# Kernel optimization log

Measured on AMD Instinct MI355X. Metric: run time of the kernel, lower is better.

The kernel has to match this reference:

```python
import jax, jax.numpy as jnp
import numpy as np

N_FEAT = 350; D = 512; L = 4; DS = 64; NREG = 6; REG_E = 32
B = 32; S = 2048
CLAMP = 20.0


def _ln(x, g, b, eps=1e-5):
    mu = jnp.mean(x, axis=-1, keepdims=True)
    var = jnp.mean(jnp.square(x - mu), axis=-1, keepdims=True)
    return (x - mu) * jax.lax.rsqrt(var + eps) * g + b


def _slstm(x, ln_g, ln_b, Wi, bi, Wf, bf, Wz, bz, Wo, bo, Wp, bp):
    # x: [B,S,D] -> out: [B,S,D]
    xn = _ln(x, ln_g, ln_b)
    log_i = jnp.clip(jnp.einsum('bsd,de->bse', xn, Wi) + bi, -CLAMP, CLAMP)
    log_f = jnp.clip(jnp.einsum('bsd,de->bse', xn, Wf) + bf, -CLAMP, CLAMP)
    z = jnp.tanh(jnp.einsum('bsd,de->bse', xn, Wz) + bz)
    o = jax.nn.sigmoid(jnp.einsum('bsd,de->bse', xn, Wo) + bo)

    def step(carry, inp):
        m, c = carry
        li, lf, zt, ot = inp
        m_new = jnp.maximum(m + lf, li)
        i_s = jnp.exp(li - m_new)
        f_s = jnp.exp(m + lf - m_new)
        c_new = f_s * c + i_s * zt
        h = ot * jnp.tanh(c_new)
        return (m_new, c_new), h

    bsz = x.shape[0]
    init = (jnp.zeros((bsz, DS), x.dtype), jnp.zeros((bsz, DS), x.dtype))
    seq = (jnp.swapaxes(log_i, 0, 1), jnp.swapaxes(log_f, 0, 1),
           jnp.swapaxes(z, 0, 1), jnp.swapaxes(o, 0, 1))
    _, hs = jax.lax.scan(step, init, seq)  # hs: [S,B,DS]
    hs = jnp.swapaxes(hs, 0, 1)  # [B,S,DS]
    return jnp.einsum('bse,ed->bsd', hs, Wp) + bp


def setup_inputs() -> dict:
    key = jax.random.key(0)
    ks = iter(jax.random.split(key, 64))
    def p(*shape):
        return jax.random.normal(next(ks), shape, dtype=jnp.float32) * 0.02
    return {
        'x': jax.random.normal(next(ks), (B, S, N_FEAT), dtype=jnp.float32),
        'regime_ids': jax.random.randint(next(ks), (B, S), 0, NREG),
        'emb_regime': p(NREG, REG_E),
        'grn_w1': p(N_FEAT + REG_E, D), 'grn_b1': jnp.zeros((D,), jnp.float32),
        'grn_w2': p(D, N_FEAT), 'grn_b2': jnp.zeros((N_FEAT,), jnp.float32),
        'in_w': p(N_FEAT, D), 'in_b': jnp.zeros((D,), jnp.float32),
        'ln_in_g': jnp.ones((L, D), jnp.float32), 'ln_in_b': jnp.zeros((L, D), jnp.float32),
        'wi': p(L, D, DS), 'bi': jnp.zeros((L, DS), jnp.float32),
        'wf': p(L, D, DS), 'bf': jnp.zeros((L, DS), jnp.float32),
        'wz': p(L, D, DS), 'bz': jnp.zeros((L, DS), jnp.float32),
        'wo': p(L, D, DS), 'bo': jnp.zeros((L, DS), jnp.float32),
        'wp': p(L, DS, D), 'bp': jnp.zeros((L, D), jnp.float32),
        'nm_g': jnp.ones((L, D), jnp.float32), 'nm_b': jnp.zeros((L, D), jnp.float32),
        'hd15_w': p(D, 1), 'hd15_b': jnp.zeros((1,), jnp.float32),
        'hd30_w': p(D, 1), 'hd30_b': jnp.zeros((1,), jnp.float32),
        'hv_w': p(D, 3), 'hv_b': jnp.zeros((3,), jnp.float32),
        'hreg_w': p(D, NREG), 'hreg_b': jnp.zeros((NREG,), jnp.float32),
        'hrng_w': p(D, 3), 'hrng_b': jnp.zeros((3,), jnp.float32),
    }


def reference(x, regime_ids, emb_regime, grn_w1, grn_b1, grn_w2, grn_b2,
              in_w, in_b, ln_in_g, ln_in_b, wi, bi, wf, bf, wz, bz, wo, bo,
              wp, bp, nm_g, nm_b, hd15_w, hd15_b, hd30_w, hd30_b,
              hv_w, hv_b, hreg_w, hreg_b, hrng_w, hrng_b):
    # Variable selection network (regime-conditioned feature weights)
    remb = emb_regime[regime_ids]                      # [B,S,32]
    comb = jnp.concatenate([x, remb], axis=-1)         # [B,S,382]
    hidden = jax.nn.elu(jnp.einsum('bsf,fd->bsd', comb, grn_w1) + grn_b1)
    weights = jax.nn.softmax(jnp.einsum('bsd,df->bsf', hidden, grn_w2) + grn_b2, axis=-1)
    xw = x * weights
    h = jnp.einsum('bsf,fd->bsd', xw, in_w) + in_b     # [B,S,D]
    for l in range(L):
        res = _slstm(h, ln_in_g[l], ln_in_b[l], wi[l], bi[l], wf[l], bf[l],
                     wz[l], bz[l], wo[l], bo[l], wp[l], bp[l])
        h = _ln(h + res, nm_g[l], nm_b[l])
    h_last = h[:, -1, :]
    return (jnp.squeeze(h_last @ hd15_w + hd15_b, -1),
            jnp.squeeze(h_last @ hd30_w + hd30_b, -1),
            h_last @ hv_w + hv_b,
            h_last @ hreg_w + hreg_b,
            h_last @ hrng_w + hrng_b,
            h_last,
            weights[:, -1, :])
```

## Files before the change

### kernel.cpp

```cpp
#include <hip/hip_runtime.h>
#include <cmath>

#define NFEAT 350
#define DMODEL 512
#define NLAYER 4
#define DSZ 64
#define REG_E 32
#define BATCH 32
#define SEQ 2048
#define MTOK (BATCH * SEQ)
#define CLAMP_V 20.0f

#define CHUNK 64
#define NCHUNK (SEQ / CHUNK)

typedef short bf16x8 __attribute__((ext_vector_type(8)));
typedef float f32x4 __attribute__((ext_vector_type(4)));

__device__ __forceinline__ unsigned short f2b(float v) {
    union { float f; unsigned int u; } x; x.f = v;
    unsigned int r = x.u + 0x7fffu + ((x.u >> 16) & 1u);
    return (unsigned short)(r >> 16);
}
__device__ __forceinline__ float b2f(unsigned short u) {
    union { unsigned int i; float f; } x; x.i = ((unsigned int)u) << 16;
    return x.f;
}
__device__ __forceinline__ unsigned int pack2(float a, float b) {
    return ((unsigned int)f2b(b) << 16) | f2b(a);
}

__global__ __launch_bounds__(256) void tconv_k(const float* __restrict__ src,
                                               unsigned short* __restrict__ dst,
                                               int K, int N, int Kpad) {
    int k = blockIdx.x * 256 + threadIdx.x;
    int n = blockIdx.y;
    if (k >= Kpad) return;
    float v = (k < K && n < N) ? src[(size_t)k * N + n] : 0.f;
    dst[(size_t)n * Kpad + k] = f2b(v);
}

__global__ __launch_bounds__(256) void tconv_g_k(const float* __restrict__ wi,
                                                 const float* __restrict__ wf,
                                                 const float* __restrict__ wz,
                                                 const float* __restrict__ wo,
                                                 unsigned short* __restrict__ dst) {
    int k = blockIdx.x * 256 + threadIdx.x;
    int n = blockIdx.y;
    int z = blockIdx.z;
    int l = z >> 2, g = z & 3;
    const float* src = (g == 0 ? wi : g == 1 ? wf : g == 2 ? wz : wo) + (size_t)l * DMODEL * DSZ;
    dst[(size_t)z * 32768 + (size_t)n * 512 + k] = f2b(src[(size_t)k * DSZ + n]);
}

__global__ __launch_bounds__(1024) void gbias_k(const float* bi, const float* bf_,
                                                const float* bz, const float* bo,
                                                float* __restrict__ gbias) {
    int t = threadIdx.x;
    int l = t >> 8, r = t & 255, g = r >> 6, e = r & 63;
    const float* s = (g == 0 ? bi : g == 1 ? bf_ : g == 2 ? bz : bo);
    gbias[t] = s[l * 64 + e];
}

__global__ __launch_bounds__(256) void build_xc_k(const float* __restrict__ x,
                                                  const int* __restrict__ rid,
                                                  const float* __restrict__ emb,
                                                  unsigned short* __restrict__ xc) {
    int i = blockIdx.x * 256 + threadIdx.x;
    int m = i / 192, p = i - m * 192;
    int k = p * 2;
    float a = 0.f, b = 0.f;
    if (k < 350) {
        const float2 v = *(const float2*)(x + (size_t)m * NFEAT + k);
        a = v.x; b = v.y;
    } else if (k < 382) {
        int r = rid[m];
        const float2 v = *(const float2*)(emb + r * REG_E + (k - 350));
        a = v.x; b = v.y;
    }
    ((unsigned int*)xc)[(size_t)m * 192 + p] = pack2(a, b);
}

template <int ALD, int EPI>
__global__ __launch_bounds__(256) void mgemm_k(const unsigned short* __restrict__ Ab,
                                               const float* __restrict__ Af,
                                               const unsigned short* __restrict__ Bt,
                                               const float* __restrict__ bias,
                                               float* __restrict__ Cf,
                                               unsigned short* __restrict__ Cb,
                                               const float* __restrict__ muA,
                                               const float* __restrict__ rstdA,
                                               const float* __restrict__ lng,
                                               const float* __restrict__ lnb,
                                               int lda, int ldb, int K, int N, int ldc) {
    __shared__ unsigned short As[128][40];
    __shared__ unsigned short Bs[128][40];
    const int tid = threadIdx.x;
    const int lane = tid & 63;
    const int wave = tid >> 6;
    const int l15 = lane & 15;
    const int quad = lane >> 4;
    const int wm = (wave >> 1) * 64;
    const int wn = (wave & 1) * 64;
    const size_t m0 = (size_t)blockIdx.y * 128;
    const int n0 = blockIdx.x * 128;

    const int sr = tid >> 2;
    const int ku = tid & 3;

    const unsigned short* Br0 = Bt + ((size_t)(n0 + sr)) * ldb + ku * 8;
    const unsigned short* Br1 = Br0 + (size_t)64 * ldb;

    const unsigned short* Ar0 = nullptr;
    const unsigned short* Ar1 = nullptr;
    const float* Fr0 = nullptr;
    const float* Fr1 = nullptr;
    float mu0 = 0.f, rs0 = 0.f, mu1 = 0.f, rs1 = 0.f;
    if (ALD == 0) {
        Ar0 = Ab + (m0 + sr) * (size_t)lda + ku * 8;
        Ar1 = Ar0 + (size_t)64 * lda;
    } else {
        Fr0 = Af + (m0 + sr) * (size_t)lda + ku * 8;
        Fr1 = Fr0 + (size_t)64 * lda;
        mu0 = muA[m0 + sr];   rs0 = rstdA[m0 + sr];
        mu1 = muA[m0 + sr + 64]; rs1 = rstdA[m0 + sr + 64];
    }

    f32x4 acc[4][4] = {};

    for (int k0 = 0; k0 < K; k0 += 32) {
        if (ALD == 0) {
            *(uint4*)&As[sr][ku * 8]      = *(const uint4*)(Ar0 + k0);
            *(uint4*)&As[sr + 64][ku * 8] = *(const uint4*)(Ar1 + k0);
        } else {
            float4 g0 = *(const float4*)(lng + k0 + ku * 8);
            float4 g1 = *(const float4*)(lng + k0 + ku * 8 + 4);
            float4 c0 = *(const float4*)(lnb + k0 + ku * 8);
            float4 c1 = *(const float4*)(lnb + k0 + ku * 8 + 4);
            {
                float4 v0 = *(const float4*)(Fr0 + k0);
                float4 v1 = *(const float4*)(Fr0 + k0 + 4);
                uint4 w;
                w.x = pack2((v0.x - mu0) * rs0 * g0.x + c0.x, (v0.y - mu0) * rs0 * g0.y + c0.y);
                w.y = pack2((v0.z - mu0) * rs0 * g0.z + c0.z, (v0.w - mu0) * rs0 * g0.w + c0.w);
                w.z = pack2((v1.x - mu0) * rs0 * g1.x + c1.x, (v1.y - mu0) * rs0 * g1.y + c1.y);
                w.w = pack2((v1.z - mu0) * rs0 * g1.z + c1.z, (v1.w - mu0) * rs0 * g1.w + c1.w);
                *(uint4*)&As[sr][ku * 8] = w;
            }
            {
                float4 v0 = *(const float4*)(Fr1 + k0);
                float4 v1 = *(const float4*)(Fr1 + k0 + 4);
                uint4 w;
                w.x = pack2((v0.x - mu1) * rs1 * g0.x + c0.x, (v0.y - mu1) * rs1 * g0.y + c0.y);
                w.y = pack2((v0.z - mu1) * rs1 * g0.z + c0.z, (v0.w - mu1) * rs1 * g0.w + c0.w);
                w.z = pack2((v1.x - mu1) * rs1 * g1.x + c1.x, (v1.y - mu1) * rs1 * g1.y + c1.y);
                w.w = pack2((v1.z - mu1) * rs1 * g1.z + c1.z, (v1.w - mu1) * rs1 * g1.w + c1.w);
                *(uint4*)&As[sr + 64][ku * 8] = w;
            }
        }
        *(uint4*)&Bs[sr][ku * 8]      = *(const uint4*)(Br0 + k0);
        *(uint4*)&Bs[sr + 64][ku * 8] = *(const uint4*)(Br1 + k0);
        __syncthreads();
        bf16x8 af[4], bf[4];
#pragma unroll
        for (int mt = 0; mt < 4; mt++)
            af[mt] = *(const bf16x8*)&As[wm + mt * 16 + l15][quad * 8];
#pragma unroll
        for (int nt = 0; nt < 4; nt++)
            bf[nt] = *(const bf16x8*)&Bs[wn + nt * 16 + l15][quad * 8];
#pragma unroll
        for (int mt = 0; mt < 4; mt++)
#pragma unroll
            for (int nt = 0; nt < 4; nt++)
                acc[mt][nt] = __builtin_amdgcn_mfma_f32_16x16x32_bf16(af[mt], bf[nt], acc[mt][nt], 0, 0, 0);
        __syncthreads();
    }

#pragma unroll
    for (int mt = 0; mt < 4; mt++) {
        int gmb = wm + mt * 16 + quad * 4;
#pragma unroll
        for (int nt = 0; nt < 4; nt++) {
            int gn = n0 + wn + nt * 16 + l15;
            if (gn < N) {
                float bv = bias[gn];
#pragma unroll
                for (int r = 0; r < 4; r++) {
                    size_t gm = m0 + gmb + r;
                    float v = acc[mt][nt][r] + bv;
                    if (EPI == 0) {
                        v = v > 0.f ? v : expm1f(v);
                        Cb[gm * (size_t)ldc + gn] = f2b(v);
                    } else if (EPI == 1) {
                        Cb[gm * (size_t)ldc + gn] = f2b(v);
                    } else if (EPI == 2) {
                        int g = gn >> 6;
                        if (g < 2) v = fminf(fmaxf(v, -CLAMP_V), CLAMP_V);
                        else if (g == 2) v = tanhf(v);
                        else v = 1.f / (1.f + expf(-v));
                        Cf[gm * (size_t)ldc + gn] = v;
                    } else {
                        Cf[gm * (size_t)ldc + gn] = v;
                    }
                }
            }
        }
    }
}

__global__ __launch_bounds__(256) void softmax_xw_k(const unsigned short* __restrict__ logits,
                                                    unsigned short* __restrict__ xc,
                                                    float* __restrict__ out_wlast) {
    int tok = blockIdx.x * 4 + (threadIdx.x >> 6);
    int lane = threadIdx.x & 63;
    const unsigned short* lr = logits + (size_t)tok * NFEAT;
    unsigned short* xr = xc + (size_t)tok * 384;
    float v[6];
    float mx = -1e30f;
#pragma unroll
    for (int i = 0; i < 6; i++) {
        int idx = lane + 64 * i;
        v[i] = (idx < NFEAT) ? b2f(lr[idx]) : -1e30f;
        mx = fmaxf(mx, v[i]);
    }
#pragma unroll
    for (int o = 32; o > 0; o >>= 1) mx = fmaxf(mx, __shfl_xor(mx, o, 64));
    float s = 0.f;
#pragma unroll
    for (int i = 0; i < 6; i++) { v[i] = expf(v[i] - mx); s += v[i]; }
#pragma unroll
    for (int o = 32; o > 0; o >>= 1) s += __shfl_xor(s, o, 64);
    float inv = 1.f / s;
    bool last = ((tok & (SEQ - 1)) == SEQ - 1);
    int b = tok >> 11;
#pragma unroll
    for (int i = 0; i < 6; i++) {
        int idx = lane + 64 * i;
        if (idx < NFEAT) {
            float w = v[i] * inv;
            xr[idx] = f2b(w * b2f(xr[idx]));
            if (last) out_wlast[b * NFEAT + idx] = w;
        } else if (idx < 352) {
            xr[idx] = 0;
        }
    }
}

__global__ __launch_bounds__(256) void ln_stats_k(const float* __restrict__ h,
                                                  float* __restrict__ mu,
                                                  float* __restrict__ rstd) {
    int tok = blockIdx.x * 4 + (threadIdx.x >> 6);
    int lane = threadIdx.x & 63;
    const float* row = h + (size_t)tok * DMODEL;
    float s = 0.f, sq = 0.f;
#pragma unroll
    for (int i = 0; i < 8; i++) {
        float v = row[lane + 64 * i];
        s += v;
        sq += v * v;
    }
#pragma unroll
    for (int o = 32; o > 0; o >>= 1) {
        s += __shfl_xor(s, o, 64);
        sq += __shfl_xor(sq, o, 64);
    }
    if (lane == 0) {
        float m = s * (1.f / DMODEL);
        float var = sq * (1.f / DMODEL) - m * m;
        mu[tok] = m;
        rstd[tok] = rsqrtf(var + 1e-5f);
    }
}

__global__ __launch_bounds__(256) void seg_agg_k(const float* __restrict__ gates,
                                                 float* __restrict__ aggF,
                                                 float* __restrict__ aggL,
                                                 float* __restrict__ aggS) {
    int b = blockIdx.x >> 3;
    int cg = blockIdx.x & 7;
    int chunk = cg * 4 + (threadIdx.x >> 6);
    int e = threadIdx.x & 63;
    const float* gp = gates + ((size_t)b * SEQ + (size_t)chunk * CHUNK) * 256;
    float F = 0.f, L = -1e30f, s = 0.f;
#pragma unroll 4
    for (int t = 0; t < CHUNK; t++) {
        const float* q = gp + (size_t)t * 256;
        float li = q[e], lf = q[64 + e], z = q[128 + e];
        float Ln = fmaxf(L + lf, li);
        s = expf(L + lf - Ln) * s + expf(li - Ln) * z;
        L = Ln;
        F += lf;
    }
    int idx = (b * NCHUNK + chunk) * 64 + e;
    aggF[idx] = F; aggL[idx] = L; aggS[idx] = s;
}

__global__ __launch_bounds__(64) void chunk_scan_k(const float* __restrict__ aggF,
                                                   const float* __restrict__ aggL,
                                                   const float* __restrict__ aggS,
                                                   float* __restrict__ stM,
                                                   float* __restrict__ stC) {
    int b = blockIdx.x;
    int e = threadIdx.x;
    float m = 0.f, c = 0.f;
    for (int k = 0; k < NCHUNK; k++) {
        int idx = (b * NCHUNK + k) * 64 + e;
        stM[idx] = m; stC[idx] = c;
        float F = aggF[idx], L = aggL[idx], s = aggS[idx];
        float mn = fmaxf(m + F, L);
        c = expf(m + F - mn) * c + expf(L - mn) * s;
        m = mn;
    }
}

__global__ __launch_bounds__(256) void replay_k(const float* __restrict__ gates,
                                                const float* __restrict__ stM,
                                                const float* __restrict__ stC,
                                                float* __restrict__ hs) {
    int b = blockIdx.x >> 3;
    int cg = blockIdx.x & 7;
    int chunk = cg * 4 + (threadIdx.x >> 6);
    int e = threadIdx.x & 63;
    int s0 = chunk * CHUNK;
    const float* gp = gates + ((size_t)b * SEQ + s0) * 256;
    float* hp = hs + ((size_t)b * SEQ + s0) * DSZ;
    int idx = (b * NCHUNK + chunk) * 64 + e;
    float m = stM[idx], c = stC[idx];
#pragma unroll 4
    for (int t = 0; t < CHUNK; t++) {
        const float* q = gp + (size_t)t * 256;
        float li = q[e], lf = q[64 + e], z = q[128 + e], o = q[192 + e];
        float mlf = m + lf;
        float mn = fmaxf(mlf, li);
        c = expf(mlf - mn) * c + expf(li - mn) * z;
        m = mn;
        hp[(size_t)t * DSZ + e] = o * tanhf(c);
    }
}

__global__ __launch_bounds__(256) void outproj_k(const float* __restrict__ hs,
                                                 const float* __restrict__ wp,
                                                 const float* __restrict__ bp,
                                                 const float* __restrict__ nmg,
                                                 const float* __restrict__ nmb,
                                                 float* __restrict__ h,
                                                 float* __restrict__ mu,
                                                 float* __restrict__ rstd) {
    __shared__ float shs[16][DSZ];
    __shared__ float swp[16][DMODEL];
    int wv = threadIdx.x >> 6;
    int lane = threadIdx.x & 63;
    int tok0 = blockIdx.x * 16;

    {
        const float4* src = (const float4*)(hs + (size_t)tok0 * DSZ);
        ((float4*)&shs[0][0])[threadIdx.x] = src[threadIdx.x];
    }
    __syncthreads();

    float acc[4][8] = {};
    for (int k0 = 0; k0 < DSZ; k0 += 16) {
        const float4* src = (const float4*)(wp + (size_t)k0 * DMODEL);
#pragma unroll
        for (int i = 0; i < 8; i++)
            ((float4*)&swp[0][0])[threadIdx.x + i * 256] = src[threadIdx.x + i * 256];
        __syncthreads();
#pragma unroll
        for (int k = 0; k < 16; k++) {
            float bv[8];
#pragma unroll
            for (int j = 0; j < 8; j++) bv[j] = swp[k][lane + 64 * j];
#pragma unroll
            for (int t = 0; t < 4; t++) {
                float av = shs[wv * 4 + t][k0 + k];
#pragma unroll
                for (int j = 0; j < 8; j++) acc[t][j] += av * bv[j];
            }
        }
        __syncthreads();
    }

#pragma unroll
    for (int t = 0; t < 4; t++) {
        int tok = tok0 + wv * 4 + t;
        float u[8];
        float s = 0.f, sq = 0.f;
#pragma unroll
        for (int j = 0; j < 8; j++) {
            int col = lane + 64 * j;
            float v = h[(size_t)tok * DMODEL + col] + acc[t][j] + bp[col];
            u[j] = v;
            s += v; sq += v * v;
        }
#pragma unroll
        for (int o = 32; o > 0; o >>= 1) { s += __shfl_xor(s, o, 64); sq += __shfl_xor(sq, o, 64); }
        float mean = s * (1.f / DMODEL);
        float var = sq * (1.f / DMODEL) - mean * mean;
        float rs = rsqrtf(var + 1e-5f);
        float s2 = 0.f, sq2 = 0.f;
#pragma unroll
        for (int j = 0; j < 8; j++) {
            int col = lane + 64 * j;
            float v = (u[j] - mean) * rs * nmg[col] + nmb[col];
            h[(size_t)tok * DMODEL + col] = v;
            s2 += v; sq2 += v * v;
        }
#pragma unroll
        for (int o = 32; o > 0; o >>= 1) { s2 += __shfl_xor(s2, o, 64); sq2 += __shfl_xor(sq2, o, 64); }
        if (lane == 0) {
            float m2 = s2 * (1.f / DMODEL);
            float v2 = sq2 * (1.f / DMODEL) - m2 * m2;
            mu[tok] = m2;
            rstd[tok] = rsqrtf(v2 + 1e-5f);
        }
    }
}

__global__ __launch_bounds__(64) void heads_k(const float* __restrict__ h,
                                              const float* hd15_w, const float* hd15_b,
                                              const float* hd30_w, const float* hd30_b,
                                              const float* hv_w, const float* hv_b,
                                              const float* hreg_w, const float* hreg_b,
                                              const float* hrng_w, const float* hrng_b,
                                              float* __restrict__ out) {
    int b = blockIdx.x;
    int lane = threadIdx.x;
    __shared__ float row[DMODEL];
    const float* hp = h + (size_t)(b * SEQ + SEQ - 1) * DMODEL;
#pragma unroll
    for (int i = 0; i < 8; i++) row[lane + 64 * i] = hp[lane + 64 * i];
    __syncthreads();
#pragma unroll
    for (int i = 0; i < 8; i++) out[448 + b * DMODEL + lane + 64 * i] = row[lane + 64 * i];
    if (lane < 14) {
        const float* w; const float* bb;
        int ncol, j, off;
        if (lane == 0)      { w = hd15_w; bb = hd15_b; ncol = 1; j = 0;         off = 0 + b; }
        else if (lane == 1) { w = hd30_w; bb = hd30_b; ncol = 1; j = 0;         off = 32 + b; }
        else if (lane < 5)  { j = lane - 2;  w = hv_w;   bb = hv_b;   ncol = 3; off = 64 + b * 3 + j; }
        else if (lane < 11) { j = lane - 5;  w = hreg_w; bb = hreg_b; ncol = 6; off = 160 + b * 6 + j; }
        else                { j = lane - 11; w = hrng_w; bb = hrng_b; ncol = 3; off = 352 + b * 3 + j; }
        float s = bb[j];
        for (int k = 0; k < DMODEL; k++) s += row[k] * w[k * ncol + j];
        out[off] = s;
    }
}

extern "C" void kernel_launch(void* const* d_in, const int* in_sizes, int n_in,
                              void* d_out, int out_size, void* d_ws, size_t ws_size,
                              hipStream_t stream) {
    (void)in_sizes; (void)n_in; (void)out_size; (void)ws_size;
    const float* x      = (const float*)d_in[0];
    const int*   rid    = (const int*)d_in[1];
    const float* emb    = (const float*)d_in[2];
    const float* grn_w1 = (const float*)d_in[3];
    const float* grn_b1 = (const float*)d_in[4];
    const float* grn_w2 = (const float*)d_in[5];
    const float* grn_b2 = (const float*)d_in[6];
    const float* in_w   = (const float*)d_in[7];
    const float* in_b   = (const float*)d_in[8];
    const float* ln_g   = (const float*)d_in[9];
    const float* ln_b   = (const float*)d_in[10];
    const float* wi     = (const float*)d_in[11];
    const float* bi     = (const float*)d_in[12];
    const float* wf     = (const float*)d_in[13];
    const float* bf_    = (const float*)d_in[14];
    const float* wz     = (const float*)d_in[15];
    const float* bz     = (const float*)d_in[16];
    const float* wo     = (const float*)d_in[17];
    const float* bo     = (const float*)d_in[18];
    const float* wp     = (const float*)d_in[19];
    const float* bp     = (const float*)d_in[20];
    const float* nm_g   = (const float*)d_in[21];
    const float* nm_b   = (const float*)d_in[22];

    float* out = (float*)d_out;
    char* W = (char*)d_ws;

    float* h               = (float*)W;
    unsigned short* hidden = (unsigned short*)W;
    unsigned short* logits = (unsigned short*)(W + 67108864);
    char* RB = W + 134217728;
    unsigned short* xc = (unsigned short*)RB;
    float* gates  = (float*)RB;
    float* hsbuf  = (float*)(RB + 67108864);
    char* RM = W + 218103808;
    float* aggF  = (float*)(RM);
    float* aggL  = (float*)(RM + 262144);
    float* aggS  = (float*)(RM + 524288);
    float* stM   = (float*)(RM + 786432);
    float* stC   = (float*)(RM + 1048576);
    float* mu    = (float*)(RM + 1310720);
    float* rstd  = (float*)(RM + 1572864);
    unsigned short* w1t  = (unsigned short*)(RM + 1835008);
    unsigned short* w2t  = (unsigned short*)(RM + 2228224);
    unsigned short* inwt = (unsigned short*)(RM + 2621440);
    unsigned short* gwt  = (unsigned short*)(RM + 2981888);
    float* gbias         = (float*)(RM + 4030464);

    build_xc_k<<<MTOK * 192 / 256, 256, 0, stream>>>(x, rid, emb, xc);
    tconv_k<<<dim3(2, 512), 256, 0, stream>>>(grn_w1, w1t, 382, 512, 384);
    tconv_k<<<dim3(2, 384), 256, 0, stream>>>(grn_w2, w2t, 512, 350, 512);
    tconv_k<<<dim3(2, 512), 256, 0, stream>>>(in_w, inwt, 350, 512, 352);
    tconv_g_k<<<dim3(2, 64, 16), 256, 0, stream>>>(wi, wf, wz, wo, gwt);
    gbias_k<<<1, 1024, 0, stream>>>(bi, bf_, bz, bo, gbias);

    mgemm_k<0, 0><<<dim3(4, 512), 256, 0, stream>>>(xc, nullptr, w1t, grn_b1, nullptr, hidden,
                                                    nullptr, nullptr, nullptr, nullptr,
                                                    384, 384, 384, 512, 512);
    mgemm_k<0, 1><<<dim3(3, 512), 256, 0, stream>>>(hidden, nullptr, w2t, grn_b2, nullptr, logits,
                                                    nullptr, nullptr, nullptr, nullptr,
                                                    512, 512, 512, 350, 350);
    softmax_xw_k<<<MTOK / 4, 256, 0, stream>>>(logits, xc, out + 16832);
    mgemm_k<0, 3><<<dim3(4, 512), 256, 0, stream>>>(xc, nullptr, inwt, in_b, h, nullptr,
                                                    nullptr, nullptr, nullptr, nullptr,
                                                    384, 352, 352, 512, 512);
    ln_stats_k<<<MTOK / 4, 256, 0, stream>>>(h, mu, rstd);

    for (int l = 0; l < NLAYER; l++) {
        mgemm_k<1, 2><<<dim3(2, 512), 256, 0, stream>>>(nullptr, h, gwt + (size_t)l * 131072,
                                                        gbias + l * 256, gates, nullptr,
                                                        mu, rstd,
                                                        ln_g + l * DMODEL, ln_b + l * DMODEL,
                                                        512, 512, 512, 256, 256);
        seg_agg_k<<<BATCH * 8, 256, 0, stream>>>(gates, aggF, aggL, aggS);
        chunk_scan_k<<<BATCH, 64, 0, stream>>>(aggF, aggL, aggS, stM, stC);
        replay_k<<<BATCH * 8, 256, 0, stream>>>(gates, stM, stC, hsbuf);

        outproj_k<<<MTOK / 16, 256, 0, stream>>>(hsbuf,
                                                 wp + (size_t)l * DSZ * DMODEL,
                                                 bp + l * DMODEL,
                                                 nm_g + l * DMODEL,
                                                 nm_b + l * DMODEL,
                                                 h, mu, rstd);
    }

    heads_k<<<BATCH, 64, 0, stream>>>(h,
                                      (const float*)d_in[23], (const float*)d_in[24],
                                      (const float*)d_in[25], (const float*)d_in[26],
                                      (const float*)d_in[27], (const float*)d_in[28],
                                      (const float*)d_in[29], (const float*)d_in[30],
                                      (const float*)d_in[31], (const float*)d_in[32],
                                      out);
}
```

Baseline: 1.445 ms.

## Use split-bf16 three-pass MFMA for gate projection with register prefetch

Replaces the LayerNorm-fused gate GEMM with a dedicated kernel that splits both the normalized activations and the gate weights into high and low bf16 parts. It accumulates three MFMA products (hh, lh, hl) to approximate fp32 precision. It also uses a 64-row tile and register prefetching of the next k-slice. The aim is to fix accuracy problems in the recurrent gates, at the cost of three times the MFMA work and double the operand traffic for this GEMM.

Result: slower. 1.483 ms (+2.6%).

```diff
diff --git a/kernel.cpp b/kernel.cpp
--- a/kernel.cpp
+++ b/kernel.cpp
@@ -44,13 +44,18 @@
                                                  const float* __restrict__ wf,
                                                  const float* __restrict__ wz,
                                                  const float* __restrict__ wo,
-                                                 unsigned short* __restrict__ dst) {
+                                                 unsigned short* __restrict__ dstH,
+                                                 unsigned short* __restrict__ dstL) {
     int k = blockIdx.x * 256 + threadIdx.x;
     int n = blockIdx.y;
     int z = blockIdx.z;
     int l = z >> 2, g = z & 3;
     const float* src = (g == 0 ? wi : g == 1 ? wf : g == 2 ? wz : wo) + (size_t)l * DMODEL * DSZ;
-    dst[(size_t)z * 32768 + (size_t)n * 512 + k] = f2b(src[(size_t)k * DSZ + n]);
+    float v = src[(size_t)k * DSZ + n];
+    unsigned short hi = f2b(v);
+    unsigned short lo = f2b(v - b2f(hi));
+    dstH[(size_t)z * 32768 + (size_t)n * 512 + k] = hi;
+    dstL[(size_t)z * 32768 + (size_t)n * 512 + k] = lo;
 }
 
 __global__ __launch_bounds__(1024) void gbias_k(const float* bi, const float* bf_,
@@ -110,54 +115,14 @@
 
     const unsigned short* Br0 = Bt + ((size_t)(n0 + sr)) * ldb + ku * 8;
     const unsigned short* Br1 = Br0 + (size_t)64 * ldb;
-
-    const unsigned short* Ar0 = nullptr;
-    const unsigned short* Ar1 = nullptr;
-    const float* Fr0 = nullptr;
-    const float* Fr1 = nullptr;
-    float mu0 = 0.f, rs0 = 0.f, mu1 = 0.f, rs1 = 0.f;
-    if (ALD == 0) {
-        Ar0 = Ab + (m0 + sr) * (size_t)lda + ku * 8;
-        Ar1 = Ar0 + (size_t)64 * lda;
-    } else {
-        Fr0 = Af + (m0 + sr) * (size_t)lda + ku * 8;
-        Fr1 = Fr0 + (size_t)64 * lda;
-        mu0 = muA[m0 + sr];   rs0 = rstdA[m0 + sr];
-        mu1 = muA[m0 + sr + 64]; rs1 = rstdA[m0 + sr + 64];
-    }
+    const unsigned short* Ar0 = Ab + (m0 + sr) * (size_t)lda + ku * 8;
+    const unsigned short* Ar1 = Ar0 + (size_t)64 * lda;
 
     f32x4 acc[4][4] = {};
 
     for (int k0 = 0; k0 < K; k0 += 32) {
-        if (ALD == 0) {
-            *(uint4*)&As[sr][ku * 8]      = *(const uint4*)(Ar0 + k0);
-            *(uint4*)&As[sr + 64][ku * 8] = *(const uint4*)(Ar1 + k0);
-        } else {
-            float4 g0 = *(const float4*)(lng + k0 + ku * 8);
-            float4 g1 = *(const float4*)(lng + k0 + ku * 8 + 4);
-            float4 c0 = *(const float4*)(lnb + k0 + ku * 8);
-            float4 c1 = *(const float4*)(lnb + k0 + ku * 8 + 4);
-            {
-                float4 v0 = *(const float4*)(Fr0 + k0);
-                float4 v1 = *(const float4*)(Fr0 + k0 + 4);
-                uint4 w;
-                w.x = pack2((v0.x - mu0) * rs0 * g0.x + c0.x, (v0.y - mu0) * rs0 * g0.y + c0.y);
-                w.y = pack2((v0.z - mu0) * rs0 * g0.z + c0.z, (v0.w - mu0) * rs0 * g0.w + c0.w);
-                w.z = pack2((v1.x - mu0) * rs0 * g1.x + c1.x, (v1.y - mu0) * rs0 * g1.y + c1.y);
-                w.w = pack2((v1.z - mu0) * rs0 * g1.z + c1.z, (v1.w - mu0) * rs0 * g1.w + c1.w);
-                *(uint4*)&As[sr][ku * 8] = w;
-            }
-            {
-                float4 v0 = *(const float4*)(Fr1 + k0);
-                float4 v1 = *(const float4*)(Fr1 + k0 + 4);
-                uint4 w;
-                w.x = pack2((v0.x - mu1) * rs1 * g0.x + c0.x, (v0.y - mu1) * rs1 * g0.y + c0.y);
-                w.y = pack2((v0.z - mu1) * rs1 * g0.z + c0.z, (v0.w - mu1) * rs1 * g0.w + c0.w);
-                w.z = pack2((v1.x - mu1) * rs1 * g1.x + c1.x, (v1.y - mu1) * rs1 * g1.y + c1.y);
-                w.w = pack2((v1.z - mu1) * rs1 * g1.z + c1.z, (v1.w - mu1) * rs1 * g1.w + c1.w);
-                *(uint4*)&As[sr + 64][ku * 8] = w;
-            }
-        }
+        *(uint4*)&As[sr][ku * 8]      = *(const uint4*)(Ar0 + k0);
+        *(uint4*)&As[sr + 64][ku * 8] = *(const uint4*)(Ar1 + k0);
         *(uint4*)&Bs[sr][ku * 8]      = *(const uint4*)(Br0 + k0);
         *(uint4*)&Bs[sr + 64][ku * 8] = *(const uint4*)(Br1 + k0);
         __syncthreads();
@@ -193,16 +158,139 @@
                         Cb[gm * (size_t)ldc + gn] = f2b(v);
                     } else if (EPI == 1) {
                         Cb[gm * (size_t)ldc + gn] = f2b(v);
-                    } else if (EPI == 2) {
-                        int g = gn >> 6;
-                        if (g < 2) v = fminf(fmaxf(v, -CLAMP_V), CLAMP_V);
-                        else if (g == 2) v = tanhf(v);
-                        else v = 1.f / (1.f + expf(-v));
-                        Cf[gm * (size_t)ldc + gn] = v;
                     } else {
                         Cf[gm * (size_t)ldc + gn] = v;
                     }
                 }
+            }
+        }
+    }
+}
+
+__global__ __launch_bounds__(256) void ggemm_k(const float* __restrict__ h,
+                                               const unsigned short* __restrict__ BtH,
+                                               const unsigned short* __restrict__ BtL,
+                                               const float* __restrict__ bias,
+                                               const float* __restrict__ mu,
+                                               const float* __restrict__ rstd,
+                                               const float* __restrict__ lng,
+                                               const float* __restrict__ lnb,
+                                               float* __restrict__ gates) {
+    __shared__ unsigned short AsH[64][40];
+    __shared__ unsigned short AsL[64][40];
+    __shared__ unsigned short BsH[128][40];
+    __shared__ unsigned short BsL[128][40];
+    const int tid = threadIdx.x;
+    const int lane = tid & 63;
+    const int wave = tid >> 6;
+    const int l15 = lane & 15;
+    const int quad = lane >> 4;
+    const int wm = (wave >> 1) * 32;
+    const int wn = (wave & 1) * 64;
+    const size_t m0 = (size_t)blockIdx.y * 64;
+    const int n0 = blockIdx.x * 128;
+
+    const int sr = tid >> 2;
+    const int ku = tid & 3;
+    const float* Ar = h + (m0 + sr) * (size_t)DMODEL + ku * 8;
+    const float muv = mu[m0 + sr];
+    const float rsv = rstd[m0 + sr];
+
+    const int br = tid >> 1;
+    const int kh = (tid & 1) * 16;
+    const unsigned short* BH = BtH + (size_t)(n0 + br) * 512 + kh;
+    const unsigned short* BL = BtL + (size_t)(n0 + br) * 512 + kh;
+
+    float4 a0 = *(const float4*)(Ar);
+    float4 a1 = *(const float4*)(Ar + 4);
+    uint4 vh0 = *(const uint4*)(BH);
+    uint4 vh1 = *(const uint4*)(BH + 8);
+    uint4 vl0 = *(const uint4*)(BL);
+    uint4 vl1 = *(const uint4*)(BL + 8);
+
+    f32x4 acc[2][4] = {};
+
+    for (int k0 = 0; k0 < DMODEL; k0 += 32) {
+        {
+            float4 g0 = *(const float4*)(lng + k0 + ku * 8);
+            float4 g1 = *(const float4*)(lng + k0 + ku * 8 + 4);
+            float4 c0 = *(const float4*)(lnb + k0 + ku * 8);
+            float4 c1 = *(const float4*)(lnb + k0 + ku * 8 + 4);
+            float v[8];
+            v[0] = (a0.x - muv) * rsv * g0.x + c0.x;
+            v[1] = (a0.y - muv) * rsv * g0.y + c0.y;
+            v[2] = (a0.z - muv) * rsv * g0.z + c0.z;
+            v[3] = (a0.w - muv) * rsv * g0.w + c0.w;
+            v[4] = (a1.x - muv) * rsv * g1.x + c1.x;
+            v[5] = (a1.y - muv) * rsv * g1.y + c1.y;
+            v[6] = (a1.z - muv) * rsv * g1.z + c1.z;
+            v[7] = (a1.w - muv) * rsv * g1.w + c1.w;
+            unsigned int hw[4], lw[4];
+#pragma unroll
+            for (int j = 0; j < 4; j++) {
+                unsigned short h0 = f2b(v[2 * j]);
+                unsigned short h1 = f2b(v[2 * j + 1]);
+                unsigned short l0 = f2b(v[2 * j] - b2f(h0));
+                unsigned short l1 = f2b(v[2 * j + 1] - b2f(h1));
+                hw[j] = (unsigned int)h0 | ((unsigned int)h1 << 16);
+                lw[j] = (unsigned int)l0 | ((unsigned int)l1 << 16);
+            }
+            *(uint4*)&AsH[sr][ku * 8] = *(uint4*)hw;
+            *(uint4*)&AsL[sr][ku * 8] = *(uint4*)lw;
+        }
+        *(uint4*)&BsH[br][kh]     = vh0;
+        *(uint4*)&BsH[br][kh + 8] = vh1;
+        *(uint4*)&BsL[br][kh]     = vl0;
+        *(uint4*)&BsL[br][kh + 8] = vl1;
+        __syncthreads();
+
+        if (k0 + 32 < DMODEL) {
+            a0 = *(const float4*)(Ar + k0 + 32);
+            a1 = *(const float4*)(Ar + k0 + 36);
+            vh0 = *(const uint4*)(BH + k0 + 32);
+            vh1 = *(const uint4*)(BH + k0 + 40);
+            vl0 = *(const uint4*)(BL + k0 + 32);
+            vl1 = *(const uint4*)(BL + k0 + 40);
+        }
+
+        bf16x8 ah[2], al[2], bh[4], bl[4];
+#pragma unroll
+        for (int mt = 0; mt < 2; mt++) {
+            ah[mt] = *(const bf16x8*)&AsH[wm + mt * 16 + l15][quad * 8];
+            al[mt] = *(const bf16x8*)&AsL[wm + mt * 16 + l15][quad * 8];
+        }
+#pragma unroll
+        for (int nt = 0; nt < 4; nt++) {
+            bh[nt] = *(const bf16x8*)&BsH[wn + nt * 16 + l15][quad * 8];
+            bl[nt] = *(const bf16x8*)&BsL[wn + nt * 16 + l15][quad * 8];
+        }
+#pragma unroll
+        for (int mt = 0; mt < 2; mt++)
+#pragma unroll
+            for (int nt = 0; nt < 4; nt++) {
+                acc[mt][nt] = __builtin_amdgcn_mfma_f32_16x16x32_bf16(ah[mt], bh[nt], acc[mt][nt], 0, 0, 0);
+                acc[mt][nt] = __builtin_amdgcn_mfma_f32_16x16x32_bf16(al[mt], bh[nt], acc[mt][nt], 0, 0, 0);
+                acc[mt][nt] = __builtin_amdgcn_mfma_f32_16x16x32_bf16(ah[mt], bl[nt], acc[mt][nt], 0, 0, 0);
+            }
+        __syncthreads();
+    }
+
+#pragma unroll
+    for (int mt = 0; mt < 2; mt++) {
+        int gmb = wm + mt * 16 + quad * 4;
+#pragma unroll
+        for (int nt = 0; nt < 4; nt++) {
+            int gn = n0 + wn + nt * 16 + l15;
+            float bv = bias[gn];
+            int g = gn >> 6;
+#pragma unroll
+            for (int r = 0; r < 4; r++) {
+                size_t gm = m0 + gmb + r;
+                float v = acc[mt][nt][r] + bv;
+                if (g < 2) v = fminf(fmaxf(v, -CLAMP_V), CLAMP_V);
+                else if (g == 2) v = tanhf(v);
+                else v = 1.f / (1.f + expf(-v));
+                gates[gm * 256 + gn] = v;
             }
         }
     }
@@ -495,14 +583,15 @@
     unsigned short* w1t  = (unsigned short*)(RM + 1835008);
     unsigned short* w2t  = (unsigned short*)(RM + 2228224);
     unsigned short* inwt = (unsigned short*)(RM + 2621440);
-    unsigned short* gwt  = (unsigned short*)(RM + 2981888);
-    float* gbias         = (float*)(RM + 4030464);
+    unsigned short* gwtH = (unsigned short*)(RM + 2981888);
+    unsigned short* gwtL = (unsigned short*)(RM + 4030464);
+    float* gbias         = (float*)(RM + 5079040);
 
     build_xc_k<<<MTOK * 192 / 256, 256, 0, stream>>>(x, rid, emb, xc);
     tconv_k<<<dim3(2, 512), 256, 0, stream>>>(grn_w1, w1t, 382, 512, 384);
     tconv_k<<<dim3(2, 384), 256, 0, stream>>>(grn_w2, w2t, 512, 350, 512);
     tconv_k<<<dim3(2, 512), 256, 0, stream>>>(in_w, inwt, 350, 512, 352);
-    tconv_g_k<<<dim3(2, 64, 16), 256, 0, stream>>>(wi, wf, wz, wo, gwt);
+    tconv_g_k<<<dim3(2, 64, 16), 256, 0, stream>>>(wi, wf, wz, wo, gwtH, gwtL);
     gbias_k<<<1, 1024, 0, stream>>>(bi, bf_, bz, bo, gbias);
 
     mgemm_k<0, 0><<<dim3(4, 512), 256, 0, stream>>>(xc, nullptr, w1t, grn_b1, nullptr, hidden,
@@ -518,11 +607,13 @@
     ln_stats_k<<<MTOK / 4, 256, 0, stream>>>(h, mu, rstd);
 
     for (int l = 0; l < NLAYER; l++) {
-        mgemm_k<1, 2><<<dim3(2, 512), 256, 0, stream>>>(nullptr, h, gwt + (size_t)l * 131072,
-                                                        gbias + l * 256, gates, nullptr,
-                                                        mu, rstd,
-                                                        ln_g + l * DMODEL, ln_b + l * DMODEL,
-                                                        512, 512, 512, 256, 256);
+        ggemm_k<<<dim3(2, 1024), 256, 0, stream>>>(h,
+                                                   gwtH + (size_t)l * 131072,
+                                                   gwtL + (size_t)l * 131072,
+                                                   gbias + l * 256,
+                                                   mu, rstd,
+                                                   ln_g + l * DMODEL, ln_b + l * DMODEL,
+                                                   gates);
         seg_agg_k<<<BATCH * 8, 256, 0, stream>>>(gates, aggF, aggL, aggS);
         chunk_scan_k<<<BATCH, 64, 0, stream>>>(aggF, aggL, aggS, stM, stC);
         replay_k<<<BATCH * 8, 256, 0, stream>>>(gates, stM, stC, hsbuf);
```
